# Performance work log

Hardware: AMD Instinct MI355X
Metric: run time of the kernel (lower is better)

The kernel has to match this reference:

```python
import jax, jax.numpy as jnp
import numpy as np

B, L, D, V = 16384, 200, 100, 100000

def setup_inputs() -> dict:
    key = jax.random.key(0)
    k1, k2 = jax.random.split(key)
    word_idxs = jax.random.randint(k1, (B, L), 0, V)  # int32 indices are fine
    # original: np.random.uniform(-1, 1, (corpus_size, embedding_dim))
    embed_table = jax.random.uniform(k2, (V, D), dtype=jnp.float32, minval=-1.0, maxval=1.0)
    weights = jnp.ones((D, 1), dtype=jnp.float32)  # torch.ones(embedding_dim).reshape(D, 1)
    return {"word_idxs": word_idxs, "embed_table": embed_table, "weights": weights}

def reference(word_idxs, embed_table, weights):
    # fused gather -> mean-pool over tokens -> dot with weights
    embeds = embed_table[word_idxs]           # [B, L, D]
    hiddens = embeds.mean(axis=1)             # [B, D]
    prod = hiddens @ weights                  # [B, 1]
    return prod
```

## Files before the change

kernel.cpp:

```cpp
#include <hip/hip_runtime.h>
#include <hip/hip_fp16.h>

#define BB 16384
#define LL 200
#define DD 100
#define VV 100000
#define CHUNK  50000
#define CI4    6250
#define NCHUNK 2
#define PBLK   256
#define PTHR   1024
#define RPW    4

__global__ __launch_bounds__(256) void rowdot_kernel(const float4* __restrict__ E4,
                                                     const float4* __restrict__ w4,
                                                     __half* __restrict__ rowdot) {
    const int tid  = blockIdx.x * blockDim.x + threadIdx.x;
    const int wave = tid >> 6;
    const int lane = threadIdx.x & 63;
    const int half = lane >> 5;
    const int sub  = lane & 31;

    float4 wv = make_float4(0.f, 0.f, 0.f, 0.f);
    if (sub < 25) wv = w4[sub];

    const int r = wave * 2 + half;
    float s = 0.0f;
    if (sub < 25) {
        float4 v = E4[(size_t)r * 25 + sub];
        s = v.x * wv.x + v.y * wv.y + v.z * wv.z + v.w * wv.w;
    }
    #pragma unroll
    for (int off = 16; off > 0; off >>= 1)
        s += __shfl_xor(s, off, 64);
    if (sub == 0) rowdot[r] = __float2half(s);
}

__global__ __launch_bounds__(1024) void pool_kernel(const int4* __restrict__ idx4,
                                                    const __half* __restrict__ rowdot,
                                                    float* __restrict__ out) {
    __shared__ __half sh[CHUNK];
    const int t    = threadIdx.x;
    const int wv   = t >> 6;
    const int lane = t & 63;
    const int row0 = blockIdx.x * 64 + wv * RPW;
    const bool act = lane < 50;

    int4 pf[RPW];
    #pragma unroll
    for (int r = 0; r < RPW; ++r)
        pf[r] = act ? idx4[(size_t)(row0 + r) * 50 + lane]
                    : make_int4(0, 0, 0, 0);

    float acc[RPW] = {0.f, 0.f, 0.f, 0.f};
    const int4* src = (const int4*)rowdot;

    #pragma unroll 1
    for (int c = 0; c < NCHUNK; ++c) {
        const int base = c * CHUNK;
        __syncthreads();
        #pragma unroll
        for (int j = 0; j < 7; ++j) {
            const int k = j * PTHR + t;
            if (k < CI4) {
                const int4* gp = src + c * CI4 + k;
                char* lb = (char*)sh + j * 16384 + wv * 1024;
                __builtin_amdgcn_global_load_lds(
                    (const __attribute__((address_space(1))) void*)gp,
                    (__attribute__((address_space(3))) void*)lb,
                    16, 0, 0);
            }
        }
        __syncthreads();
        if (act) {
            #pragma unroll
            for (int r = 0; r < RPW; ++r) {
                int4 i4 = pf[r];
                int a0 = i4.x - base, a1 = i4.y - base;
                int a2 = i4.z - base, a3 = i4.w - base;
                if ((unsigned)a0 < (unsigned)CHUNK) acc[r] += __half2float(sh[a0]);
                if ((unsigned)a1 < (unsigned)CHUNK) acc[r] += __half2float(sh[a1]);
                if ((unsigned)a2 < (unsigned)CHUNK) acc[r] += __half2float(sh[a2]);
                if ((unsigned)a3 < (unsigned)CHUNK) acc[r] += __half2float(sh[a3]);
            }
        }
    }

    #pragma unroll
    for (int r = 0; r < RPW; ++r) {
        float s = acc[r];
        #pragma unroll
        for (int off = 32; off > 0; off >>= 1)
            s += __shfl_xor(s, off, 64);
        if (lane == 0) out[row0 + r] = s * (1.0f / LL);
    }
}

extern "C" void kernel_launch(void* const* d_in, const int* in_sizes, int n_in,
                              void* d_out, int out_size, void* d_ws, size_t ws_size,
                              hipStream_t stream) {
    const int4*   idx4   = (const int4*)d_in[0];
    const float4* E4     = (const float4*)d_in[1];
    const float4* w4     = (const float4*)d_in[2];
    float*        out    = (float*)d_out;
    __half*       rowdot = (__half*)d_ws;

    rowdot_kernel<<<VV / 8, 256, 0, stream>>>(E4, w4, rowdot);
    pool_kernel<<<PBLK, PTHR, 0, stream>>>(idx4, rowdot, out);
}
```

Measured before the change: 21.78 us.

## Fuse rowdot and pooling kernels with a device-wide atomic barrier

Merges the table-projection kernel and the pooling kernel into one persistent launch of 256 blocks. Each block first computes a slice of the per-row dot products (two rows per wave, packed half2 stores), then all blocks meet at a global atomic spin barrier before the chunked LDS gather-and-sum. This removes the second kernel launch and its inter-kernel gap, and overlaps the index prefetch with the projection. In exchange it adds a hipMemsetAsync per call, relies on all 256 blocks being co-resident to avoid deadlock, and the projection now runs on far fewer waves than the old 12500-block launch.

```diff
diff --git a/kernel.cpp b/kernel.cpp
--- a/kernel.cpp
+++ b/kernel.cpp
@@ -8,43 +8,25 @@
 #define CHUNK  50000
 #define CI4    6250
 #define NCHUNK 2
-#define PBLK   256
-#define PTHR   1024
+#define FBLK   256
+#define FTHR   1024
 #define RPW    4
+#define PAIRS_PER_BLK 196
 
-__global__ __launch_bounds__(256) void rowdot_kernel(const float4* __restrict__ E4,
+__global__ __launch_bounds__(1024) void fused_kernel(const int4* __restrict__ idx4,
+                                                     const float4* __restrict__ E4,
                                                      const float4* __restrict__ w4,
-                                                     __half* __restrict__ rowdot) {
-    const int tid  = blockIdx.x * blockDim.x + threadIdx.x;
-    const int wave = tid >> 6;
-    const int lane = threadIdx.x & 63;
-    const int half = lane >> 5;
-    const int sub  = lane & 31;
-
-    float4 wv = make_float4(0.f, 0.f, 0.f, 0.f);
-    if (sub < 25) wv = w4[sub];
-
-    const int r = wave * 2 + half;
-    float s = 0.0f;
-    if (sub < 25) {
-        float4 v = E4[(size_t)r * 25 + sub];
-        s = v.x * wv.x + v.y * wv.y + v.z * wv.z + v.w * wv.w;
-    }
-    #pragma unroll
-    for (int off = 16; off > 0; off >>= 1)
-        s += __shfl_xor(s, off, 64);
-    if (sub == 0) rowdot[r] = __float2half(s);
-}
-
-__global__ __launch_bounds__(1024) void pool_kernel(const int4* __restrict__ idx4,
-                                                    const __half* __restrict__ rowdot,
-                                                    float* __restrict__ out) {
+                                                     __half* __restrict__ rowdot,
+                                                     int* __restrict__ bar,
+                                                     float* __restrict__ out) {
     __shared__ __half sh[CHUNK];
     const int t    = threadIdx.x;
     const int wv   = t >> 6;
     const int lane = t & 63;
+    const int half = lane >> 5;
+    const int sub  = lane & 31;
+    const bool act = lane < 50;
     const int row0 = blockIdx.x * 64 + wv * RPW;
-    const bool act = lane < 50;
 
     int4 pf[RPW];
     #pragma unroll
@@ -52,16 +34,49 @@
         pf[r] = act ? idx4[(size_t)(row0 + r) * 50 + lane]
                     : make_int4(0, 0, 0, 0);
 
+    float4 wvf = make_float4(0.f, 0.f, 0.f, 0.f);
+    if (sub < 25) wvf = w4[sub];
+    const int p0 = blockIdx.x * PAIRS_PER_BLK;
+    #pragma unroll 1
+    for (int i = wv; i < PAIRS_PER_BLK; i += 16) {
+        const int p = p0 + i;
+        if (p < VV / 2) {
+            const int r = p * 2 + half;
+            float s = 0.0f;
+            if (sub < 25) {
+                float4 v = E4[(size_t)r * 25 + sub];
+                s = v.x * wvf.x + v.y * wvf.y + v.z * wvf.z + v.w * wvf.w;
+            }
+            #pragma unroll
+            for (int off = 16; off > 0; off >>= 1)
+                s += __shfl_xor(s, off, 64);
+            float s1 = __shfl(s, 32, 64);
+            if (lane == 0) {
+                unsigned u0 = __half_as_ushort(__float2half(s));
+                unsigned u1 = __half_as_ushort(__float2half(s1));
+                ((unsigned*)rowdot)[p] = u0 | (u1 << 16);
+            }
+        }
+    }
+
+    __syncthreads();
+    if (t == 0) {
+        __hip_atomic_fetch_add(bar, 1, __ATOMIC_RELEASE, __HIP_MEMORY_SCOPE_AGENT);
+        while (__hip_atomic_load(bar, __ATOMIC_ACQUIRE, __HIP_MEMORY_SCOPE_AGENT) < FBLK)
+            __builtin_amdgcn_s_sleep(2);
+        __threadfence();
+    }
+    __syncthreads();
+
     float acc[RPW] = {0.f, 0.f, 0.f, 0.f};
     const int4* src = (const int4*)rowdot;
-
     #pragma unroll 1
     for (int c = 0; c < NCHUNK; ++c) {
         const int base = c * CHUNK;
         __syncthreads();
         #pragma unroll
         for (int j = 0; j < 7; ++j) {
-            const int k = j * PTHR + t;
+            const int k = j * FTHR + t;
             if (k < CI4) {
                 const int4* gp = src + c * CI4 + k;
                 char* lb = (char*)sh + j * 16384 + wv * 1024;
@@ -104,7 +119,8 @@
     const float4* w4     = (const float4*)d_in[2];
     float*        out    = (float*)d_out;
     __half*       rowdot = (__half*)d_ws;
+    int*          bar    = (int*)((char*)d_ws + 262144);
 
-    rowdot_kernel<<<VV / 8, 256, 0, stream>>>(E4, w4, rowdot);
-    pool_kernel<<<PBLK, PTHR, 0, stream>>>(idx4, rowdot, out);
+    hipMemsetAsync(bar, 0, sizeof(int), stream);
+    fused_kernel<<<FBLK, FTHR, 0, stream>>>(idx4, E4, w4, rowdot, bar, out);
 }
```

Result: slower. 43.19 us (+98.3%).
